# Kernel optimization log

Measured on AMD Instinct MI355X. Metric: run time of the kernel, lower is better.

Reference implementation:

```python
import jax, jax.numpy as jnp
import numpy as np

DIM_IN = 64
DIM_OUT = 64
SCALE = DIM_IN ** (-0.5)

def setup_inputs() -> dict:
    key = jax.random.key(0)
    ks = jax.random.split(key, 9)
    B, C, N, S = 4, DIM_IN, 16384, 16
    inp = {
        "xyz": jax.random.normal(ks[0], (B, 3, N), jnp.float32),
        "neighbor_xyz": jax.random.normal(ks[1], (B, 3, N, S), jnp.float32),
        "point": jax.random.normal(ks[2], (B, C, N), jnp.float32),
        "neighbor_points": jax.random.normal(ks[3], (B, C, N, S), jnp.float32),
        "neighbor_cost": jax.random.normal(ks[4], (B, C, N, S), jnp.float32),
        # 1x1 conv weights (kernel dims squeezed): [out_ch, in_ch]
        "w_k": jax.random.normal(ks[5], (DIM_IN, DIM_IN), jnp.float32) * (DIM_IN ** -0.5),
        "w_v": jax.random.normal(ks[6], (DIM_OUT, DIM_IN), jnp.float32) * (DIM_IN ** -0.5),
        "w_pos": jax.random.normal(ks[7], (DIM_IN, 4), jnp.float32) * 0.5,
        "b_pos": jax.random.normal(ks[8], (DIM_IN,), jnp.float32) * 0.01,
    }
    return inp

def reference(xyz, neighbor_xyz, point, neighbor_points, neighbor_cost, w_k, w_v, w_pos, b_pos):
    # xyz: [B,3,N]; neighbor_xyz: [B,3,N,S]; point: [B,C,N]; neighbor_cost: [B,C,N,S]
    tmp = xyz[:, :, :, None] - neighbor_xyz                      # [B,3,N,S]
    xyz_norm = jnp.linalg.norm(tmp, axis=1, keepdims=True)       # [B,1,N,S]
    pos = jnp.concatenate([tmp, xyz_norm], axis=1)               # [B,4,N,S]
    pos_enc = jnp.einsum('oc,bcns->bons', w_pos, pos) + b_pos[None, :, None, None]
    k = jnp.einsum('oc,bcns->bons', w_k, neighbor_cost + pos_enc)  # [B,C,N,S]
    v = jnp.einsum('oc,bcns->bons', w_v, neighbor_cost)            # [B,Co,N,S]
    q = point * SCALE                                              # note: self.q conv unused in original
    attn = jnp.einsum('bcn,bcns->bns', q, k)                       # channel-reduced scores
    attn = jax.nn.softmax(attn, axis=-1)                           # softmax over S neighbors
    out = jnp.einsum('bns,bcns->bcn', attn, v)                     # [B,Co,N]
    return out
```

## Files before the change

### kernel.cpp

```cpp
#include <hip/hip_runtime.h>

#define NCH    64
#define NPTS   16384
#define NS     16
#define NB     4
#define QSCALE 0.125f

__global__ __launch_bounds__(256) void pt_attn_kernel(
    const float* __restrict__ xyz,
    const float* __restrict__ nxyz,
    const float* __restrict__ point,
    const float* __restrict__ cost,
    const float* __restrict__ w_k,
    const float* __restrict__ w_v,
    const float* __restrict__ w_pos,
    const float* __restrict__ b_pos,
    float* __restrict__ out)
{
    const int wave = (blockIdx.x * blockDim.x + threadIdx.x) >> 6;
    const int lane = threadIdx.x & 63;
    const int tilesPerB = NPTS / 64;
    const int b = wave / tilesPerB;
    const int n = (wave % tilesPerB) * 64 + lane;

    const float* point_b = point + b * NCH * NPTS;
    const float* cost_b  = cost  + (size_t)b * NCH * NPTS * NS;
    const float* xyz_b   = xyz   + b * 3 * NPTS;
    const float* nxyz_b  = nxyz  + b * 3 * NPTS * NS;

    float qp[NCH];
#pragma unroll
    for (int c = 0; c < NCH; ++c) qp[c] = 0.f;
    for (int o = 0; o < NCH; ++o) {
        float qo = point_b[o * NPTS + n] * QSCALE;
#pragma unroll
        for (int c = 0; c < NCH; ++c)
            qp[c] = fmaf(w_k[o * NCH + c], qo, qp[c]);
    }

    float qs0 = 0.f, qs1 = 0.f, qs2 = 0.f, qs3 = 0.f, qb = 0.f;
#pragma unroll
    for (int c = 0; c < NCH; ++c) {
        qs0 = fmaf(qp[c], w_pos[c * 4 + 0], qs0);
        qs1 = fmaf(qp[c], w_pos[c * 4 + 1], qs1);
        qs2 = fmaf(qp[c], w_pos[c * 4 + 2], qs2);
        qs3 = fmaf(qp[c], w_pos[c * 4 + 3], qs3);
        qb  = fmaf(qp[c], b_pos[c], qb);
    }

    float lg[NS];
    {
        float x0 = xyz_b[0 * NPTS + n];
        float x1 = xyz_b[1 * NPTS + n];
        float x2 = xyz_b[2 * NPTS + n];
        const float4* g0 = (const float4*)(nxyz_b + (0 * NPTS + n) * NS);
        const float4* g1 = (const float4*)(nxyz_b + (1 * NPTS + n) * NS);
        const float4* g2 = (const float4*)(nxyz_b + (2 * NPTS + n) * NS);
#pragma unroll
        for (int s4 = 0; s4 < 4; ++s4) {
            float4 a0 = g0[s4], a1 = g1[s4], a2 = g2[s4];
            float t0, t1, t2, nr;
            t0 = x0 - a0.x; t1 = x1 - a1.x; t2 = x2 - a2.x;
            nr = sqrtf(t0 * t0 + t1 * t1 + t2 * t2);
            lg[s4 * 4 + 0] = fmaf(qs0, t0, fmaf(qs1, t1, fmaf(qs2, t2, fmaf(qs3, nr, qb))));
            t0 = x0 - a0.y; t1 = x1 - a1.y; t2 = x2 - a2.y;
            nr = sqrtf(t0 * t0 + t1 * t1 + t2 * t2);
            lg[s4 * 4 + 1] = fmaf(qs0, t0, fmaf(qs1, t1, fmaf(qs2, t2, fmaf(qs3, nr, qb))));
            t0 = x0 - a0.z; t1 = x1 - a1.z; t2 = x2 - a2.z;
            nr = sqrtf(t0 * t0 + t1 * t1 + t2 * t2);
            lg[s4 * 4 + 2] = fmaf(qs0, t0, fmaf(qs1, t1, fmaf(qs2, t2, fmaf(qs3, nr, qb))));
            t0 = x0 - a0.w; t1 = x1 - a1.w; t2 = x2 - a2.w;
            nr = sqrtf(t0 * t0 + t1 * t1 + t2 * t2);
            lg[s4 * 4 + 3] = fmaf(qs0, t0, fmaf(qs1, t1, fmaf(qs2, t2, fmaf(qs3, nr, qb))));
        }
    }

#pragma unroll
    for (int c = 0; c < NCH; ++c) {
        const float4* cp = (const float4*)(cost_b + (c * NPTS + n) * NS);
        float4 v0 = cp[0], v1 = cp[1], v2 = cp[2], v3 = cp[3];
        float qc = qp[c];
        lg[0]  = fmaf(qc, v0.x, lg[0]);  lg[1]  = fmaf(qc, v0.y, lg[1]);
        lg[2]  = fmaf(qc, v0.z, lg[2]);  lg[3]  = fmaf(qc, v0.w, lg[3]);
        lg[4]  = fmaf(qc, v1.x, lg[4]);  lg[5]  = fmaf(qc, v1.y, lg[5]);
        lg[6]  = fmaf(qc, v1.z, lg[6]);  lg[7]  = fmaf(qc, v1.w, lg[7]);
        lg[8]  = fmaf(qc, v2.x, lg[8]);  lg[9]  = fmaf(qc, v2.y, lg[9]);
        lg[10] = fmaf(qc, v2.z, lg[10]); lg[11] = fmaf(qc, v2.w, lg[11]);
        lg[12] = fmaf(qc, v3.x, lg[12]); lg[13] = fmaf(qc, v3.y, lg[13]);
        lg[14] = fmaf(qc, v3.z, lg[14]); lg[15] = fmaf(qc, v3.w, lg[15]);
    }

    float m = lg[0];
#pragma unroll
    for (int s = 1; s < NS; ++s) m = fmaxf(m, lg[s]);
    float at[NS];
    float Z = 0.f;
#pragma unroll
    for (int s = 0; s < NS; ++s) { at[s] = __expf(lg[s] - m); Z += at[s]; }
    float rz = 1.f / Z;
#pragma unroll
    for (int s = 0; s < NS; ++s) at[s] *= rz;

    float wc[NCH];
#pragma unroll
    for (int c = 0; c < NCH; ++c) {
        const float4* cp = (const float4*)(cost_b + (c * NPTS + n) * NS);
        float4 v0 = cp[0], v1 = cp[1], v2 = cp[2], v3 = cp[3];
        float a;
        a = at[0] * v0.x;
        a = fmaf(at[1],  v0.y, a); a = fmaf(at[2],  v0.z, a); a = fmaf(at[3],  v0.w, a);
        a = fmaf(at[4],  v1.x, a); a = fmaf(at[5],  v1.y, a); a = fmaf(at[6],  v1.z, a);
        a = fmaf(at[7],  v1.w, a); a = fmaf(at[8],  v2.x, a); a = fmaf(at[9],  v2.y, a);
        a = fmaf(at[10], v2.z, a); a = fmaf(at[11], v2.w, a); a = fmaf(at[12], v3.x, a);
        a = fmaf(at[13], v3.y, a); a = fmaf(at[14], v3.z, a); a = fmaf(at[15], v3.w, a);
        wc[c] = a;
    }

    float* out_b = out + b * NCH * NPTS;
    for (int o = 0; o < NCH; ++o) {
        const float* wvr = w_v + o * NCH;
        float acc = 0.f;
#pragma unroll
        for (int c = 0; c < NCH; ++c)
            acc = fmaf(wvr[c], wc[c], acc);
        out_b[o * NPTS + n] = acc;
    }
}

extern "C" void kernel_launch(void* const* d_in, const int* in_sizes, int n_in,
                              void* d_out, int out_size, void* d_ws, size_t ws_size,
                              hipStream_t stream) {
    const float* xyz   = (const float*)d_in[0];
    const float* nxyz  = (const float*)d_in[1];
    const float* point = (const float*)d_in[2];
    const float* cost  = (const float*)d_in[4];
    const float* w_k   = (const float*)d_in[5];
    const float* w_v   = (const float*)d_in[6];
    const float* w_pos = (const float*)d_in[7];
    const float* b_pos = (const float*)d_in[8];
    float* outp = (float*)d_out;

    dim3 grid(256), block(256);
    hipLaunchKernelGGL(pt_attn_kernel, grid, block, 0, stream,
                       xyz, nxyz, point, cost, w_k, w_v, w_pos, b_pos, outp);
}
```

Measured before the change: 615.5 us.

## Split each point across four threads with shared-memory stages for projections

```diff
diff --git a/kernel.cpp b/kernel.cpp
--- a/kernel.cpp
+++ b/kernel.cpp
@@ -3,7 +3,6 @@
 #define NCH    64
 #define NPTS   16384
 #define NS     16
-#define NB     4
 #define QSCALE 0.125f
 
 __global__ __launch_bounds__(256) void pt_attn_kernel(
@@ -17,113 +16,141 @@
     const float* __restrict__ b_pos,
     float* __restrict__ out)
 {
-    const int wave = (blockIdx.x * blockDim.x + threadIdx.x) >> 6;
-    const int lane = threadIdx.x & 63;
-    const int tilesPerB = NPTS / 64;
-    const int b = wave / tilesPerB;
-    const int n = (wave % tilesPerB) * 64 + lane;
+    __shared__ float ptwc[NCH][64];
+    __shared__ float qp[NCH][64];
+    __shared__ float qg[5][64];
 
-    const float* point_b = point + b * NCH * NPTS;
+    const int t  = threadIdx.x;
+    const int b  = blockIdx.x >> 8;
+    const int n0 = (blockIdx.x & 255) << 6;
+
+    const float* point_b = point + (size_t)b * NCH * NPTS;
     const float* cost_b  = cost  + (size_t)b * NCH * NPTS * NS;
-    const float* xyz_b   = xyz   + b * 3 * NPTS;
-    const float* nxyz_b  = nxyz  + b * 3 * NPTS * NS;
+    const float* xyz_b   = xyz   + (size_t)b * 3 * NPTS;
+    const float* nxyz_b  = nxyz  + (size_t)b * 3 * NPTS * NS;
+    float*       out_b   = out   + (size_t)b * NCH * NPTS;
 
-    float qp[NCH];
 #pragma unroll
-    for (int c = 0; c < NCH; ++c) qp[c] = 0.f;
-    for (int o = 0; o < NCH; ++o) {
-        float qo = point_b[o * NPTS + n] * QSCALE;
+    for (int i = 0; i < 16; ++i) {
+        int flat = t + i * 256;
+        int o = flat >> 6, n = flat & 63;
+        ((float*)ptwc)[flat] = point_b[o * NPTS + n0 + n] * QSCALE;
+    }
+    __syncthreads();
+
+    {
+        const int w = t >> 6, lane = t & 63;
+        const int cbase = w * 16;
+        float acc[16];
 #pragma unroll
-        for (int c = 0; c < NCH; ++c)
-            qp[c] = fmaf(w_k[o * NCH + c], qo, qp[c]);
+        for (int j = 0; j < 16; ++j) acc[j] = 0.f;
+#pragma unroll 4
+        for (int o = 0; o < NCH; ++o) {
+            float pv = ptwc[o][lane];
+            const float* wkr = w_k + o * NCH + cbase;
+#pragma unroll
+            for (int j = 0; j < 16; ++j)
+                acc[j] = fmaf(wkr[j], pv, acc[j]);
+        }
+#pragma unroll
+        for (int j = 0; j < 16; ++j)
+            qp[cbase + j][lane] = acc[j];
     }
+    __syncthreads();
 
-    float qs0 = 0.f, qs1 = 0.f, qs2 = 0.f, qs3 = 0.f, qb = 0.f;
-#pragma unroll
-    for (int c = 0; c < NCH; ++c) {
-        qs0 = fmaf(qp[c], w_pos[c * 4 + 0], qs0);
-        qs1 = fmaf(qp[c], w_pos[c * 4 + 1], qs1);
-        qs2 = fmaf(qp[c], w_pos[c * 4 + 2], qs2);
-        qs3 = fmaf(qp[c], w_pos[c * 4 + 3], qs3);
-        qb  = fmaf(qp[c], b_pos[c], qb);
+    {
+        const int n = t & 63, j = t >> 6;
+        float a = 0.f, ab = 0.f;
+#pragma unroll 8
+        for (int c = 0; c < NCH; ++c) {
+            float q = qp[c][n];
+            a = fmaf(q, w_pos[c * 4 + j], a);
+            if (j == 0) ab = fmaf(q, b_pos[c], ab);
+        }
+        qg[j][n] = a;
+        if (j == 0) qg[4][n] = ab;
     }
+    __syncthreads();
 
-    float lg[NS];
+    const int s4 = t & 3, nl = t >> 2;
+    const int n  = n0 + nl;
+    const float4* costp = (const float4*)(cost_b + (size_t)n * NS) + s4;
+
+    float4 lg;
     {
         float x0 = xyz_b[0 * NPTS + n];
         float x1 = xyz_b[1 * NPTS + n];
         float x2 = xyz_b[2 * NPTS + n];
-        const float4* g0 = (const float4*)(nxyz_b + (0 * NPTS + n) * NS);
-        const float4* g1 = (const float4*)(nxyz_b + (1 * NPTS + n) * NS);
-        const float4* g2 = (const float4*)(nxyz_b + (2 * NPTS + n) * NS);
-#pragma unroll
-        for (int s4 = 0; s4 < 4; ++s4) {
-            float4 a0 = g0[s4], a1 = g1[s4], a2 = g2[s4];
-            float t0, t1, t2, nr;
-            t0 = x0 - a0.x; t1 = x1 - a1.x; t2 = x2 - a2.x;
-            nr = sqrtf(t0 * t0 + t1 * t1 + t2 * t2);
-            lg[s4 * 4 + 0] = fmaf(qs0, t0, fmaf(qs1, t1, fmaf(qs2, t2, fmaf(qs3, nr, qb))));
-            t0 = x0 - a0.y; t1 = x1 - a1.y; t2 = x2 - a2.y;
-            nr = sqrtf(t0 * t0 + t1 * t1 + t2 * t2);
-            lg[s4 * 4 + 1] = fmaf(qs0, t0, fmaf(qs1, t1, fmaf(qs2, t2, fmaf(qs3, nr, qb))));
-            t0 = x0 - a0.z; t1 = x1 - a1.z; t2 = x2 - a2.z;
-            nr = sqrtf(t0 * t0 + t1 * t1 + t2 * t2);
-            lg[s4 * 4 + 2] = fmaf(qs0, t0, fmaf(qs1, t1, fmaf(qs2, t2, fmaf(qs3, nr, qb))));
-            t0 = x0 - a0.w; t1 = x1 - a1.w; t2 = x2 - a2.w;
-            nr = sqrtf(t0 * t0 + t1 * t1 + t2 * t2);
-            lg[s4 * 4 + 3] = fmaf(qs0, t0, fmaf(qs1, t1, fmaf(qs2, t2, fmaf(qs3, nr, qb))));
-        }
+        float4 a0 = *(const float4*)(nxyz_b + (size_t)(0 * NPTS + n) * NS + s4 * 4);
+        float4 a1 = *(const float4*)(nxyz_b + (size_t)(1 * NPTS + n) * NS + s4 * 4);
+        float4 a2 = *(const float4*)(nxyz_b + (size_t)(2 * NPTS + n) * NS + s4 * 4);
+        float qs0 = qg[0][nl], qs1 = qg[1][nl], qs2 = qg[2][nl];
+        float qs3 = qg[3][nl], qb  = qg[4][nl];
+        float t0, t1, t2, nr;
+        t0 = x0 - a0.x; t1 = x1 - a1.x; t2 = x2 - a2.x;
+        nr = sqrtf(fmaf(t0, t0, fmaf(t1, t1, t2 * t2)));
+        lg.x = fmaf(qs0, t0, fmaf(qs1, t1, fmaf(qs2, t2, fmaf(qs3, nr, qb))));
+        t0 = x0 - a0.y; t1 = x1 - a1.y; t2 = x2 - a2.y;
+        nr = sqrtf(fmaf(t0, t0, fmaf(t1, t1, t2 * t2)));
+        lg.y = fmaf(qs0, t0, fmaf(qs1, t1, fmaf(qs2, t2, fmaf(qs3, nr, qb))));
+        t0 = x0 - a0.z; t1 = x1 - a1.z; t2 = x2 - a2.z;
+        nr = sqrtf(fmaf(t0, t0, fmaf(t1, t1, t2 * t2)));
+        lg.z = fmaf(qs0, t0, fmaf(qs1, t1, fmaf(qs2, t2, fmaf(qs3, nr, qb))));
+        t0 = x0 - a0.w; t1 = x1 - a1.w; t2 = x2 - a2.w;
+        nr = sqrtf(fmaf(t0, t0, fmaf(t1, t1, t2 * t2)));
+        lg.w = fmaf(qs0, t0, fmaf(qs1, t1, fmaf(qs2, t2, fmaf(qs3, nr, qb))));
     }
 
-#pragma unroll
+#pragma unroll 8
     for (int c = 0; c < NCH; ++c) {
-        const float4* cp = (const float4*)(cost_b + (c * NPTS + n) * NS);
-        float4 v0 = cp[0], v1 = cp[1], v2 = cp[2], v3 = cp[3];
-        float qc = qp[c];
-        lg[0]  = fmaf(qc, v0.x, lg[0]);  lg[1]  = fmaf(qc, v0.y, lg[1]);
-        lg[2]  = fmaf(qc, v0.z, lg[2]);  lg[3]  = fmaf(qc, v0.w, lg[3]);
-        lg[4]  = fmaf(qc, v1.x, lg[4]);  lg[5]  = fmaf(qc, v1.y, lg[5]);
-        lg[6]  = fmaf(qc, v1.z, lg[6]);  lg[7]  = fmaf(qc, v1.w, lg[7]);
-        lg[8]  = fmaf(qc, v2.x, lg[8]);  lg[9]  = fmaf(qc, v2.y, lg[9]);
-        lg[10] = fmaf(qc, v2.z, lg[10]); lg[11] = fmaf(qc, v2.w, lg[11]);
-        lg[12] = fmaf(qc, v3.x, lg[12]); lg[13] = fmaf(qc, v3.y, lg[13]);
-        lg[14] = fmaf(qc, v3.z, lg[14]); lg[15] = fmaf(qc, v3.w, lg[15]);
+        float4 cv = costp[(size_t)c * NPTS * 4];
+        float qc = qp[c][nl];
+        lg.x = fmaf(qc, cv.x, lg.x);
+        lg.y = fmaf(qc, cv.y, lg.y);
+        lg.z = fmaf(qc, cv.z, lg.z);
+        lg.w = fmaf(qc, cv.w, lg.w);
     }
 
-    float m = lg[0];
+    float m = fmaxf(fmaxf(lg.x, lg.y), fmaxf(lg.z, lg.w));
+    m = fmaxf(m, __shfl_xor(m, 1));
+    m = fmaxf(m, __shfl_xor(m, 2));
+    float4 at;
+    at.x = __expf(lg.x - m);
+    at.y = __expf(lg.y - m);
+    at.z = __expf(lg.z - m);
+    at.w = __expf(lg.w - m);
+    float Z = at.x + at.y + at.z + at.w;
+    Z += __shfl_xor(Z, 1);
+    Z += __shfl_xor(Z, 2);
+    float rz = 1.f / Z;
+    at.x *= rz; at.y *= rz; at.z *= rz; at.w *= rz;
+
+#pragma unroll 8
+    for (int c = 0; c < NCH; ++c) {
+        float4 cv = costp[(size_t)c * NPTS * 4];
+        float p = fmaf(at.x, cv.x, fmaf(at.y, cv.y, fmaf(at.z, cv.z, at.w * cv.w)));
+        p += __shfl_xor(p, 1);
+        p += __shfl_xor(p, 2);
+        if (s4 == 0) ptwc[c][nl] = p;
+    }
+    __syncthreads();
+
+    {
+        const int w = t >> 6, lane = t & 63;
+        const int obase = w * 16;
+        float acc[16];
 #pragma unroll
-    for (int s = 1; s < NS; ++s) m = fmaxf(m, lg[s]);
-    float at[NS];
-    float Z = 0.f;
+        for (int j = 0; j < 16; ++j) acc[j] = 0.f;
+#pragma unroll 4
+        for (int c = 0; c < NCH; ++c) {
+            float wv = ptwc[c][lane];
 #pragma unroll
-    for (int s = 0; s < NS; ++s) { at[s] = __expf(lg[s] - m); Z += at[s]; }
-    float rz = 1.f / Z;
+            for (int j = 0; j < 16; ++j)
+                acc[j] = fmaf(w_v[(obase + j) * NCH + c], wv, acc[j]);
+        }
 #pragma unroll
-    for (int s = 0; s < NS; ++s) at[s] *= rz;
-
-    float wc[NCH];
-#pragma unroll
-    for (int c = 0; c < NCH; ++c) {
-        const float4* cp = (const float4*)(cost_b + (c * NPTS + n) * NS);
-        float4 v0 = cp[0], v1 = cp[1], v2 = cp[2], v3 = cp[3];
-        float a;
-        a = at[0] * v0.x;
-        a = fmaf(at[1],  v0.y, a); a = fmaf(at[2],  v0.z, a); a = fmaf(at[3],  v0.w, a);
-        a = fmaf(at[4],  v1.x, a); a = fmaf(at[5],  v1.y, a); a = fmaf(at[6],  v1.z, a);
-        a = fmaf(at[7],  v1.w, a); a = fmaf(at[8],  v2.x, a); a = fmaf(at[9],  v2.y, a);
-        a = fmaf(at[10], v2.z, a); a = fmaf(at[11], v2.w, a); a = fmaf(at[12], v3.x, a);
-        a = fmaf(at[13], v3.y, a); a = fmaf(at[14], v3.z, a); a = fmaf(at[15], v3.w, a);
-        wc[c] = a;
-    }
-
-    float* out_b = out + b * NCH * NPTS;
-    for (int o = 0; o < NCH; ++o) {
-        const float* wvr = w_v + o * NCH;
-        float acc = 0.f;
-#pragma unroll
-        for (int c = 0; c < NCH; ++c)
-            acc = fmaf(wvr[c], wc[c], acc);
-        out_b[o * NPTS + n] = acc;
+        for (int j = 0; j < 16; ++j)
+            out_b[(obase + j) * NPTS + n0 + lane] = acc[j];
     }
 }
 
@@ -140,7 +167,7 @@
     const float* b_pos = (const float*)d_in[8];
     float* outp = (float*)d_out;
 
-    dim3 grid(256), block(256);
+    dim3 grid(1024), block(256);
     hipLaunchKernelGGL(pt_attn_kernel, grid, block, 0, stream,
                        xyz, nxyz, point, cost, w_k, w_v, w_pos, b_pos, outp);
 }
```

After: 570.6 us. 1.08x faster.
